# Kernel tuning notes

Hardware: AMD Instinct MI355X
Metric: run time of the kernel (lower is better)

Reference implementation:

```python
import jax, jax.numpy as jnp
import numpy as np

B, S, C, H = 8, 1024, 768, 8
D = C // H  # head dim = 96
MLP = 4 * C


def setup_inputs() -> dict:
    key = jax.random.key(0)
    ks = jax.random.split(key, 12)
    sc = 0.02
    return {
        "x": jax.random.normal(ks[0], (B, S, C), jnp.float32),
        "ln1_w": jnp.ones((S, C), jnp.float32),
        "ln1_b": jnp.zeros((S, C), jnp.float32),
        "ln2_w": jnp.ones((S, C), jnp.float32),
        "ln2_b": jnp.zeros((S, C), jnp.float32),
        "qkv_w": jax.random.normal(ks[1], (C, 3 * C), jnp.float32) * sc,
        "proj_w": jax.random.normal(ks[2], (C, C), jnp.float32) * sc,
        "mlp_w1": jax.random.normal(ks[3], (C, MLP), jnp.float32) * sc,
        "mlp_b1": jnp.zeros((MLP,), jnp.float32),
        "mlp_w2": jax.random.normal(ks[4], (MLP, C), jnp.float32) * sc,
        "mlp_b2": jnp.zeros((C,), jnp.float32),
    }


def _layernorm2d(x, w, b, eps=1e-5):
    # normalizes over BOTH (seq, channel) dims, per nn.LayerNorm([length, channel])
    mu = jnp.mean(x, axis=(-2, -1), keepdims=True)
    var = jnp.mean(jnp.square(x - mu), axis=(-2, -1), keepdims=True)
    return (x - mu) * jax.lax.rsqrt(var + eps) * w + b


def _attention(x, qkv_w, proj_w):
    b, s, _ = x.shape
    qkv = (x @ qkv_w).reshape(b, s, 3, H, D)
    q, k, v = qkv[:, :, 0], qkv[:, :, 1], qkv[:, :, 2]  # [b, s, h, d]
    # NOTE: original module applies NO 1/sqrt(d) scaling
    scores = jnp.einsum("bshd,bthd->bhst", q, k)
    attn = jax.nn.softmax(scores, axis=-1)
    out = jnp.einsum("bhst,bthd->bshd", attn, v).reshape(b, s, C)
    return out @ proj_w


def reference(x, ln1_w, ln1_b, ln2_w, ln2_b, qkv_w, proj_w, mlp_w1, mlp_b1, mlp_w2, mlp_b2):
    # dropout is identity in eval mode
    h = x + _attention(_layernorm2d(x, ln1_w, ln1_b), qkv_w, proj_w)
    y = _layernorm2d(h, ln2_w, ln2_b)
    y = jax.nn.gelu(y @ mlp_w1 + mlp_b1, approximate=False)
    return h + (y @ mlp_w2 + mlp_b2)
```

## Files before the change

### kernel.cpp

```cpp
#include <hip/hip_runtime.h>
#include <hip/hip_bf16.h>

#define S_LEN 1024
#define NB 8
#define NC 768
#define NH 8
#define HD 96
#define NMLP 3072
#define SC (S_LEN*NC)
#define BS (NB*S_LEN)

typedef __attribute__((ext_vector_type(8))) unsigned short u16x8;
typedef __attribute__((ext_vector_type(4))) unsigned short u16x4;
typedef __attribute__((ext_vector_type(8))) __bf16 bf16x8;
typedef __attribute__((ext_vector_type(4))) float f32x4;

__device__ __forceinline__ unsigned short f2b(float f) {
  union { __hip_bfloat16 h; unsigned short u; } cvt;
  cvt.h = __float2bfloat16(f);
  return cvt.u;
}

__device__ __forceinline__ void gload16(const unsigned short* g, unsigned short* l) {
  __builtin_amdgcn_global_load_lds(
      (const __attribute__((address_space(1))) unsigned int*)g,
      (__attribute__((address_space(3))) unsigned int*)l, 16, 0, 0);
}

template<int EPI>
__global__ __launch_bounds__(256, 2)
void gemm_bt(const unsigned short* __restrict__ A, int lda,
             const unsigned short* __restrict__ Bt, int ldb,
             void* __restrict__ Cv, int ldc,
             int K,
             const float* __restrict__ bias,
             const float* __restrict__ residual, int ldr)
{
  __shared__ unsigned short As[128*32];
  __shared__ unsigned short Bs[128*32];
  const int tid = threadIdx.x;
  const int lane = tid & 63;
  const int wid = tid >> 6;
  const int wm = wid & 1, wn = wid >> 1;
  const int r15 = lane & 15, g = lane >> 4;
  const int tm = blockIdx.x * 128;
  const int tn = blockIdx.y * 128;

  const unsigned short* Ab = A  + (size_t)(tm + wid*32 + (lane>>2))*lda + (lane&3)*8;
  const unsigned short* Bb = Bt + (size_t)(tn + wid*32 + (lane>>2))*ldb + (lane&3)*8;

  f32x4 acc[4][4];
  #pragma unroll
  for (int m = 0; m < 4; ++m)
    #pragma unroll
    for (int n = 0; n < 4; ++n)
      acc[m][n] = (f32x4){0.f, 0.f, 0.f, 0.f};

  for (int k0 = 0; k0 < K; k0 += 32) {
    gload16(Ab + k0,                    As + (wid*2 + 0)*512);
    gload16(Ab + (size_t)16*lda + k0,   As + (wid*2 + 1)*512);
    gload16(Bb + k0,                    Bs + (wid*2 + 0)*512);
    gload16(Bb + (size_t)16*ldb + k0,   Bs + (wid*2 + 1)*512);
    __syncthreads();
    bf16x8 af[4], bfr[4];
    #pragma unroll
    for (int m = 0; m < 4; ++m)
      af[m] = *(const bf16x8*)(As + (wm*64 + m*16 + r15)*32 + g*8);
    #pragma unroll
    for (int n = 0; n < 4; ++n)
      bfr[n] = *(const bf16x8*)(Bs + (wn*64 + n*16 + r15)*32 + g*8);
    #pragma unroll
    for (int m = 0; m < 4; ++m)
      #pragma unroll
      for (int n = 0; n < 4; ++n)
        acc[m][n] = __builtin_amdgcn_mfma_f32_16x16x32_bf16(af[m], bfr[n], acc[m][n], 0, 0, 0);
    __syncthreads();
  }

  unsigned short* Cu = (unsigned short*)Cv;
  float* Cf = (float*)Cv;
  #pragma unroll
  for (int m = 0; m < 4; ++m) {
    #pragma unroll
    for (int n = 0; n < 4; ++n) {
      const int col = tn + wn*64 + n*16 + r15;
      #pragma unroll
      for (int r = 0; r < 4; ++r) {
        const int row = tm + wm*64 + m*16 + g*4 + r;
        float v = acc[m][n][r];
        if (EPI == 2 || EPI == 4) v += bias[col];
        if (EPI == 3 || EPI == 4) v += residual[(size_t)row*ldr + col];
        if (EPI == 2) v = 0.5f*v*(1.0f + erff(v*0.70710678118654752f));
        if (EPI == 0 || EPI == 2) Cu[(size_t)row*ldc + col] = f2b(v);
        else                      Cf[(size_t)row*ldc + col] = v;
      }
    }
  }
}

__global__ __launch_bounds__(256, 2)
void flash_attn(const unsigned short* __restrict__ qkv,
                const unsigned short* __restrict__ vt,
                unsigned short* __restrict__ outb)
{
  __shared__ unsigned short Ks[128*96];
  __shared__ unsigned short Vs[96*128];
  __shared__ unsigned short Ps[128*128];
  const int tid = threadIdx.x, lane = tid & 63, wq = tid >> 6;
  const int r15 = lane & 15, g = lane >> 4;
  const int bh = blockIdx.y, b = bh >> 3, h = bh & 7;
  const int q0 = blockIdx.x * 128;
  const int swz = (r15 & 7) << 4;
  char* PsB = (char*)Ps;
  char* VsB = (char*)Vs;

  bf16x8 qf[2][3];
  {
    const unsigned short* qb = qkv + ((size_t)b*S_LEN + q0 + wq*32 + r15)*2304 + h*HD + g*8;
    #pragma unroll
    for (int n = 0; n < 2; ++n)
      #pragma unroll
      for (int kc = 0; kc < 3; ++kc)
        qf[n][kc] = *(const bf16x8*)(qb + (size_t)n*16*2304 + kc*32);
  }

  int krow[6], kcol[6], vrow[6], vcol[6];
  #pragma unroll
  for (int i = 0; i < 6; ++i) {
    const int c = (wq*6 + i)*64 + lane;
    krow[i] = c / 12;
    kcol[i] = (c % 12) * 8;
    const int L = c * 16;
    const int row = L >> 8, cb = L & 255;
    vrow[i] = row;
    vcol[i] = (cb ^ ((row & 7) << 4)) >> 1;
  }
  const unsigned short* kbase = qkv + (size_t)b*S_LEN*2304 + NC + h*HD;
  const unsigned short* vbase = vt + (size_t)bh*HD*S_LEN;

  f32x4 oacc[6][2];
  #pragma unroll
  for (int m = 0; m < 6; ++m) {
    oacc[m][0] = (f32x4){0.f,0.f,0.f,0.f};
    oacc[m][1] = (f32x4){0.f,0.f,0.f,0.f};
  }
  float mrun[2] = {-INFINITY, -INFINITY};
  float lrun[2] = {0.f, 0.f};

  for (int kt = 0; kt < 8; ++kt) {
    const unsigned short* ksrc = kbase + (size_t)kt*128*2304;
    const unsigned short* vsrc = vbase + kt*128;
    #pragma unroll
    for (int i = 0; i < 6; ++i) {
      gload16(ksrc + (size_t)krow[i]*2304 + kcol[i], Ks + (wq*6 + i)*512);
      gload16(vsrc + vrow[i]*1024 + vcol[i],         Vs + (wq*6 + i)*512);
    }
    __syncthreads();

    f32x4 sacc[8][2];
    #pragma unroll
    for (int m = 0; m < 8; ++m) {
      sacc[m][0] = (f32x4){0.f,0.f,0.f,0.f};
      sacc[m][1] = (f32x4){0.f,0.f,0.f,0.f};
    }
    #pragma unroll
    for (int kc = 0; kc < 3; ++kc)
      #pragma unroll
      for (int m = 0; m < 8; ++m) {
        bf16x8 kf = *(const bf16x8*)(Ks + (m*16 + r15)*96 + kc*32 + g*8);
        sacc[m][0] = __builtin_amdgcn_mfma_f32_16x16x32_bf16(kf, qf[0][kc], sacc[m][0], 0,0,0);
        sacc[m][1] = __builtin_amdgcn_mfma_f32_16x16x32_bf16(kf, qf[1][kc], sacc[m][1], 0,0,0);
      }

    #pragma unroll
    for (int n = 0; n < 2; ++n) {
      float pm = -INFINITY;
      #pragma unroll
      for (int m = 0; m < 8; ++m)
        #pragma unroll
        for (int r = 0; r < 4; ++r) pm = fmaxf(pm, sacc[m][n][r]);
      pm = fmaxf(pm, __shfl_xor(pm, 16));
      pm = fmaxf(pm, __shfl_xor(pm, 32));
      const float newm = fmaxf(mrun[n], pm);
      const float scale = __expf(mrun[n] - newm);
      mrun[n] = newm;
      const int qloc = wq*32 + n*16 + r15;
      float s = 0.f;
      #pragma unroll
      for (int m = 0; m < 8; ++m) {
        float e0 = __expf(sacc[m][n][0] - newm);
        float e1 = __expf(sacc[m][n][1] - newm);
        float e2 = __expf(sacc[m][n][2] - newm);
        float e3 = __expf(sacc[m][n][3] - newm);
        s += (e0 + e1) + (e2 + e3);
        u16x4 pk = { f2b(e0), f2b(e1), f2b(e2), f2b(e3) };
        *(u16x4*)(PsB + ((qloc*256 + m*32 + g*8) ^ swz)) = pk;
      }
      s += __shfl_xor(s, 16);
      s += __shfl_xor(s, 32);
      lrun[n] = lrun[n]*scale + s;
      #pragma unroll
      for (int m = 0; m < 6; ++m) oacc[m][n] *= scale;
    }

    #pragma unroll
    for (int kc = 0; kc < 4; ++kc) {
      bf16x8 pf0 = *(const bf16x8*)(PsB + (((wq*32      + r15)*256 + kc*64 + g*16) ^ swz));
      bf16x8 pf1 = *(const bf16x8*)(PsB + (((wq*32 + 16 + r15)*256 + kc*64 + g*16) ^ swz));
      #pragma unroll
      for (int m = 0; m < 6; ++m) {
        bf16x8 vf = *(const bf16x8*)(VsB + (((m*16 + r15)*256 + kc*64 + g*16) ^ swz));
        oacc[m][0] = __builtin_amdgcn_mfma_f32_16x16x32_bf16(vf, pf0, oacc[m][0], 0,0,0);
        oacc[m][1] = __builtin_amdgcn_mfma_f32_16x16x32_bf16(vf, pf1, oacc[m][1], 0,0,0);
      }
    }
    __syncthreads();
  }

  #pragma unroll
  for (int n = 0; n < 2; ++n) {
    const float inv = 1.0f / lrun[n];
    unsigned short* orow = outb + ((size_t)b*S_LEN + q0 + wq*32 + n*16 + r15)*NC + h*HD;
    #pragma unroll
    for (int m = 0; m < 6; ++m) {
      u16x4 pk = { f2b(oacc[m][n][0]*inv), f2b(oacc[m][n][1]*inv),
                   f2b(oacc[m][n][2]*inv), f2b(oacc[m][n][3]*inv) };
      *(u16x4*)(orow + m*16 + g*4) = pk;
    }
  }
}

__global__ void transpose_cast(const float* __restrict__ W, unsigned short* __restrict__ Wt,
                               int K, int N)
{
  __shared__ float tile[32][33];
  const int tx = threadIdx.x & 31, ty = threadIdx.x >> 5;
  const int n0 = blockIdx.x * 32, k0 = blockIdx.y * 32;
  #pragma unroll
  for (int i = 0; i < 32; i += 8)
    tile[ty + i][tx] = W[(size_t)(k0 + ty + i)*N + n0 + tx];
  __syncthreads();
  #pragma unroll
  for (int i = 0; i < 32; i += 8)
    Wt[(size_t)(n0 + ty + i)*K + k0 + tx] = f2b(tile[tx][ty + i]);
}

__global__ void transpose_v(const unsigned short* __restrict__ qkv, unsigned short* __restrict__ vt)
{
  __shared__ unsigned short tile[32][33];
  const int bh = blockIdx.z, b = bh >> 3, h = bh & 7;
  const unsigned short* v = qkv + (size_t)b*S_LEN*3*NC + 2*NC + h*HD;
  unsigned short* o = vt + (size_t)bh*HD*S_LEN;
  const int s0 = blockIdx.x * 32, d0 = blockIdx.y * 32;
  const int tx = threadIdx.x & 31, ty = threadIdx.x >> 5;
  #pragma unroll
  for (int i = 0; i < 32; i += 8)
    tile[ty + i][tx] = v[(size_t)(s0 + ty + i)*(3*NC) + d0 + tx];
  __syncthreads();
  #pragma unroll
  for (int i = 0; i < 32; i += 8)
    o[(size_t)(d0 + ty + i)*S_LEN + s0 + tx] = tile[tx][ty + i];
}

__global__ void ln_part(const float* __restrict__ X, float* __restrict__ part)
{
  const int b = blockIdx.x / 96, blk = blockIdx.x % 96;
  const float4* xb = (const float4*)(X + (size_t)b*SC);
  float s = 0.f, s2 = 0.f;
  #pragma unroll
  for (int i = 0; i < 8; ++i) {
    float4 v = xb[blk*2048 + i*256 + threadIdx.x];
    s  += v.x + v.y + v.z + v.w;
    s2 += v.x*v.x + v.y*v.y + v.z*v.z + v.w*v.w;
  }
  #pragma unroll
  for (int o = 32; o; o >>= 1) { s += __shfl_down(s, o); s2 += __shfl_down(s2, o); }
  __shared__ float r1[4], r2[4];
  const int w = threadIdx.x >> 6;
  if ((threadIdx.x & 63) == 0) { r1[w] = s; r2[w] = s2; }
  __syncthreads();
  if (threadIdx.x == 0) {
    part[(b*96 + blk)*2]     = r1[0] + r1[1] + r1[2] + r1[3];
    part[(b*96 + blk)*2 + 1] = r2[0] + r2[1] + r2[2] + r2[3];
  }
}

__global__ void ln_fin(const float* __restrict__ part, float* __restrict__ stats)
{
  const int b = blockIdx.x;
  float s = 0.f, s2 = 0.f;
  for (int i = threadIdx.x; i < 96; i += 64) {
    s  += part[(b*96 + i)*2];
    s2 += part[(b*96 + i)*2 + 1];
  }
  #pragma unroll
  for (int o = 32; o; o >>= 1) { s += __shfl_down(s, o); s2 += __shfl_down(s2, o); }
  if (threadIdx.x == 0) {
    const float inv = 1.0f / (float)SC;
    const float mu = s * inv;
    const float var = s2 * inv - mu*mu;
    stats[b*2] = mu;
    stats[b*2 + 1] = rsqrtf(var + 1e-5f);
  }
}

__global__ void ln_apply(const float* __restrict__ X, const float* __restrict__ W,
                         const float* __restrict__ Bv, const float* __restrict__ stats,
                         unsigned short* __restrict__ out)
{
  const size_t i = ((size_t)blockIdx.x*256 + threadIdx.x) * 8;
  const int b = (int)(i / SC);
  const size_t r = i % SC;
  const float mu = stats[b*2], rs = stats[b*2 + 1];
  float4 x0 = *(const float4*)(X + i),  x1 = *(const float4*)(X + i + 4);
  float4 w0 = *(const float4*)(W + r),  w1 = *(const float4*)(W + r + 4);
  float4 b0 = *(const float4*)(Bv + r), b1 = *(const float4*)(Bv + r + 4);
  u16x8 o;
  o[0] = f2b((x0.x - mu)*rs*w0.x + b0.x);
  o[1] = f2b((x0.y - mu)*rs*w0.y + b0.y);
  o[2] = f2b((x0.z - mu)*rs*w0.z + b0.z);
  o[3] = f2b((x0.w - mu)*rs*w0.w + b0.w);
  o[4] = f2b((x1.x - mu)*rs*w1.x + b1.x);
  o[5] = f2b((x1.y - mu)*rs*w1.y + b1.y);
  o[6] = f2b((x1.z - mu)*rs*w1.z + b1.z);
  o[7] = f2b((x1.w - mu)*rs*w1.w + b1.w);
  *(u16x8*)(out + i) = o;
}

extern "C" void kernel_launch(void* const* d_in, const int* in_sizes, int n_in,
                              void* d_out, int out_size, void* d_ws, size_t ws_size,
                              hipStream_t stream) {
  const float* x      = (const float*)d_in[0];
  const float* ln1_w  = (const float*)d_in[1];
  const float* ln1_b  = (const float*)d_in[2];
  const float* ln2_w  = (const float*)d_in[3];
  const float* ln2_b  = (const float*)d_in[4];
  const float* qkv_w  = (const float*)d_in[5];
  const float* proj_w = (const float*)d_in[6];
  const float* mlp_w1 = (const float*)d_in[7];
  const float* mlp_b1 = (const float*)d_in[8];
  const float* mlp_w2 = (const float*)d_in[9];
  const float* mlp_b2 = (const float*)d_in[10];
  float* out = (float*)d_out;

  char* ws = (char*)d_ws;
  size_t off = 0;
  auto alloc = [&](size_t b) { size_t o = off; off += (b + 255) & ~(size_t)255; return o; };
  unsigned short* wqkvT  = (unsigned short*)(ws + alloc((size_t)3*NC*NC*2));
  unsigned short* wprojT = (unsigned short*)(ws + alloc((size_t)NC*NC*2));
  unsigned short* w1T    = (unsigned short*)(ws + alloc((size_t)NMLP*NC*2));
  unsigned short* w2T    = (unsigned short*)(ws + alloc((size_t)NC*NMLP*2));
  unsigned short* lnbf   = (unsigned short*)(ws + alloc((size_t)BS*NC*2));
  const size_t qkvOff    = alloc((size_t)BS*3*NC*2);
  unsigned short* qkvbf  = (unsigned short*)(ws + qkvOff);
  unsigned short* vt     = (unsigned short*)(ws + alloc((size_t)NB*NH*HD*S_LEN*2));
  unsigned short* ybf    = (unsigned short*)(ws + qkvOff);
  float* hbuf            = (float*)(ws + alloc((size_t)BS*NC*4));
  float* part            = (float*)(ws + alloc((size_t)NB*96*2*4));
  float* stats           = (float*)(ws + alloc((size_t)NB*2*4));
  (void)ws_size; (void)in_sizes; (void)n_in; (void)out_size;

  const dim3 blk(256);

  transpose_cast<<<dim3(3*NC/32, NC/32),   blk, 0, stream>>>(qkv_w,  wqkvT,  NC, 3*NC);
  transpose_cast<<<dim3(NC/32, NC/32),     blk, 0, stream>>>(proj_w, wprojT, NC, NC);
  transpose_cast<<<dim3(NMLP/32, NC/32),   blk, 0, stream>>>(mlp_w1, w1T,    NC, NMLP);
  transpose_cast<<<dim3(NC/32, NMLP/32),   blk, 0, stream>>>(mlp_w2, w2T,    NMLP, NC);

  ln_part<<<dim3(NB*96), blk, 0, stream>>>(x, part);
  ln_fin<<<dim3(NB), dim3(64), 0, stream>>>(part, stats);
  ln_apply<<<dim3(BS*NC/2048), blk, 0, stream>>>(x, ln1_w, ln1_b, stats, lnbf);

  gemm_bt<0><<<dim3(BS/128, 3*NC/128), blk, 0, stream>>>(
      lnbf, NC, wqkvT, NC, qkvbf, 3*NC, NC, nullptr, nullptr, 0);

  transpose_v<<<dim3(S_LEN/32, HD/32, NB*NH), blk, 0, stream>>>(qkvbf, vt);

  flash_attn<<<dim3(S_LEN/128, NB*NH), blk, 0, stream>>>(qkvbf, vt, lnbf);

  gemm_bt<3><<<dim3(BS/128, NC/128), blk, 0, stream>>>(
      lnbf, NC, wprojT, NC, hbuf, NC, NC, nullptr, x, NC);

  ln_part<<<dim3(NB*96), blk, 0, stream>>>(hbuf, part);
  ln_fin<<<dim3(NB), dim3(64), 0, stream>>>(part, stats);
  ln_apply<<<dim3(BS*NC/2048), blk, 0, stream>>>(hbuf, ln2_w, ln2_b, stats, lnbf);

  gemm_bt<2><<<dim3(BS/128, NMLP/128), blk, 0, stream>>>(
      lnbf, NC, w1T, NC, ybf, NMLP, NC, mlp_b1, nullptr, 0);

  gemm_bt<4><<<dim3(BS/128, NC/128), blk, 0, stream>>>(
      ybf, NMLP, w2T, NMLP, out, NC, NMLP, mlp_b2, hbuf, NC);
}
```

Before: 298.9 us.

## Replace GEMM with 8-wave 128x256 triple-buffered pipelined kernel and tanh GELU

Replaces the single-buffered 128x128 GEMM with a 512-thread kernel on a 128x256 tile and K-steps of 64. It uses a three-stage LDS ring with XOR-swizzled layout, and staggers global-to-LDS prefetches between MFMA groups under s_setprio. This is meant to hide global load latency and LDS bank conflicts, and to drop one barrier per K step. The erf-based GELU epilogue becomes a tanh approximation, and flash attention MFMA loops gain setprio hints. The trade-offs are more LDS use, one block per CU, and slight numeric deviation from exact GELU.

Result: slower. 325.0 us (+8.7%).

```diff
diff --git a/kernel.cpp b/kernel.cpp
--- a/kernel.cpp
+++ b/kernel.cpp
@@ -27,27 +27,48 @@
       (__attribute__((address_space(3))) unsigned int*)l, 16, 0, 0);
 }
 
+__device__ __forceinline__ float gelu_f(float v) {
+  float u = v * (0.7978845608f + 0.0356774081f * v * v);
+  float au = fabsf(u);
+  float e = __expf(-2.0f * au);
+  float th = (1.0f - e) / (1.0f + e);
+  th = copysignf(th, u);
+  return 0.5f * v * (1.0f + th);
+}
+
 template<int EPI>
-__global__ __launch_bounds__(256, 2)
-void gemm_bt(const unsigned short* __restrict__ A, int lda,
-             const unsigned short* __restrict__ Bt, int ldb,
-             void* __restrict__ Cv, int ldc,
-             int K,
-             const float* __restrict__ bias,
-             const float* __restrict__ residual, int ldr)
-{
-  __shared__ unsigned short As[128*32];
-  __shared__ unsigned short Bs[128*32];
-  const int tid = threadIdx.x;
-  const int lane = tid & 63;
-  const int wid = tid >> 6;
+__global__ __launch_bounds__(512, 1)
+void gemm8(const unsigned short* __restrict__ A, int lda,
+           const unsigned short* __restrict__ Bt, int ldb,
+           void* __restrict__ Cv, int ldc, int K,
+           const float* __restrict__ bias,
+           const float* __restrict__ residual, int ldr)
+{
+  __shared__ unsigned short As[3*8192];
+  __shared__ unsigned short Bs[3*16384];
+  const int tid = threadIdx.x, lane = tid & 63, wid = tid >> 6;
   const int wm = wid & 1, wn = wid >> 1;
   const int r15 = lane & 15, g = lane >> 4;
-  const int tm = blockIdx.x * 128;
-  const int tn = blockIdx.y * 128;
-
-  const unsigned short* Ab = A  + (size_t)(tm + wid*32 + (lane>>2))*lda + (lane&3)*8;
-  const unsigned short* Bb = Bt + (size_t)(tn + wid*32 + (lane>>2))*ldb + (lane&3)*8;
+  const int tm = blockIdx.x * 128, tn = blockIdx.y * 256;
+  const int NT = K >> 6;
+
+  const int srow = lane >> 3;
+  const int scol = ((lane & 7) ^ srow) << 3;
+  const unsigned short* Ag = A  + (size_t)(tm + wid*8 + srow)*lda + scol;
+  const unsigned short* Bg = Bt + (size_t)(tn + wid*8 + srow)*ldb + scol;
+
+  const int kx  = (r15 & 7) << 4;
+  const int k0b = (g*16) ^ kx;
+  const int k1b = (64 + g*16) ^ kx;
+  char* AsB = (char*)As;
+  char* BsB = (char*)Bs;
+  const int arow = (wm*64 + r15) * 128;
+  const int brow = (wn*64 + r15) * 128;
+
+#define LDA8(m,ks) (*(const bf16x8*)(AsB + bufA + arow + (m)*2048 + ((ks) ? k1b : k0b)))
+#define LDB8(n,ks) (*(const bf16x8*)(BsB + bufB + brow + (n)*2048 + ((ks) ? k1b : k0b)))
+#define STGA(j,kk,bf) gload16(Ag + (size_t)((j)*64)*lda + (kk), As + (bf)*8192  + (j)*4096 + wid*512)
+#define STGB(j,kk,bf) gload16(Bg + (size_t)((j)*64)*ldb + (kk), Bs + (bf)*16384 + (j)*4096 + wid*512)
 
   f32x4 acc[4][4];
   #pragma unroll
@@ -56,26 +77,80 @@
     for (int n = 0; n < 4; ++n)
       acc[m][n] = (f32x4){0.f, 0.f, 0.f, 0.f};
 
-  for (int k0 = 0; k0 < K; k0 += 32) {
-    gload16(Ab + k0,                    As + (wid*2 + 0)*512);
-    gload16(Ab + (size_t)16*lda + k0,   As + (wid*2 + 1)*512);
-    gload16(Bb + k0,                    Bs + (wid*2 + 0)*512);
-    gload16(Bb + (size_t)16*ldb + k0,   Bs + (wid*2 + 1)*512);
-    __syncthreads();
-    bf16x8 af[4], bfr[4];
-    #pragma unroll
-    for (int m = 0; m < 4; ++m)
-      af[m] = *(const bf16x8*)(As + (wm*64 + m*16 + r15)*32 + g*8);
-    #pragma unroll
-    for (int n = 0; n < 4; ++n)
-      bfr[n] = *(const bf16x8*)(Bs + (wn*64 + n*16 + r15)*32 + g*8);
-    #pragma unroll
-    for (int m = 0; m < 4; ++m)
-      #pragma unroll
-      for (int n = 0; n < 4; ++n)
-        acc[m][n] = __builtin_amdgcn_mfma_f32_16x16x32_bf16(af[m], bfr[n], acc[m][n], 0, 0, 0);
-    __syncthreads();
-  }
+  STGA(0,0,0); STGA(1,0,0); STGB(0,0,0); STGB(1,0,0); STGB(2,0,0); STGB(3,0,0);
+  STGA(0,64,1); STGA(1,64,1); STGB(0,64,1); STGB(1,64,1); STGB(2,64,1); STGB(3,64,1);
+  asm volatile("s_waitcnt vmcnt(6)" ::: "memory");
+  __builtin_amdgcn_s_barrier();
+
+  int buf = 0, nbuf = 2;
+  for (int t = 0; t < NT; ++t) {
+    const int kk = (t + 2) << 6;
+    const bool pre = (t + 2) < NT;
+    const int bufA = buf * 16384;
+    const int bufB = buf * 32768;
+    bf16x8 a0[2][2], a1[2][2], b0[2][2], b1[2][2];
+
+    if (pre) { STGA(0,kk,nbuf); STGA(1,kk,nbuf); }
+    #pragma unroll
+    for (int m = 0; m < 2; ++m) { a0[m][0] = LDA8(m,0); a0[m][1] = LDA8(m,1); }
+    #pragma unroll
+    for (int n = 0; n < 2; ++n) { b0[n][0] = LDB8(n,0); b0[n][1] = LDB8(n,1); }
+    __builtin_amdgcn_s_setprio(1);
+    #pragma unroll
+    for (int m = 0; m < 2; ++m)
+      #pragma unroll
+      for (int n = 0; n < 2; ++n) {
+        acc[m][n] = __builtin_amdgcn_mfma_f32_16x16x32_bf16(a0[m][0], b0[n][0], acc[m][n], 0,0,0);
+        acc[m][n] = __builtin_amdgcn_mfma_f32_16x16x32_bf16(a0[m][1], b0[n][1], acc[m][n], 0,0,0);
+      }
+    __builtin_amdgcn_s_setprio(0);
+
+    if (pre) { STGB(0,kk,nbuf); STGB(1,kk,nbuf); }
+    #pragma unroll
+    for (int n = 0; n < 2; ++n) { b1[n][0] = LDB8(n+2,0); b1[n][1] = LDB8(n+2,1); }
+    __builtin_amdgcn_s_setprio(1);
+    #pragma unroll
+    for (int m = 0; m < 2; ++m)
+      #pragma unroll
+      for (int n = 0; n < 2; ++n) {
+        acc[m][n+2] = __builtin_amdgcn_mfma_f32_16x16x32_bf16(a0[m][0], b1[n][0], acc[m][n+2], 0,0,0);
+        acc[m][n+2] = __builtin_amdgcn_mfma_f32_16x16x32_bf16(a0[m][1], b1[n][1], acc[m][n+2], 0,0,0);
+      }
+    __builtin_amdgcn_s_setprio(0);
+
+    if (pre) { STGB(2,kk,nbuf); STGB(3,kk,nbuf); }
+    #pragma unroll
+    for (int m = 0; m < 2; ++m) { a1[m][0] = LDA8(m+2,0); a1[m][1] = LDA8(m+2,1); }
+    __builtin_amdgcn_s_setprio(1);
+    #pragma unroll
+    for (int m = 0; m < 2; ++m)
+      #pragma unroll
+      for (int n = 0; n < 2; ++n) {
+        acc[m+2][n+2] = __builtin_amdgcn_mfma_f32_16x16x32_bf16(a1[m][0], b1[n][0], acc[m+2][n+2], 0,0,0);
+        acc[m+2][n+2] = __builtin_amdgcn_mfma_f32_16x16x32_bf16(a1[m][1], b1[n][1], acc[m+2][n+2], 0,0,0);
+      }
+    __builtin_amdgcn_s_setprio(0);
+
+    __builtin_amdgcn_s_setprio(1);
+    #pragma unroll
+    for (int m = 0; m < 2; ++m)
+      #pragma unroll
+      for (int n = 0; n < 2; ++n) {
+        acc[m+2][n] = __builtin_amdgcn_mfma_f32_16x16x32_bf16(a1[m][0], b0[n][0], acc[m+2][n], 0,0,0);
+        acc[m+2][n] = __builtin_amdgcn_mfma_f32_16x16x32_bf16(a1[m][1], b0[n][1], acc[m+2][n], 0,0,0);
+      }
+    __builtin_amdgcn_s_setprio(0);
+
+    if (pre) asm volatile("s_waitcnt vmcnt(6)" ::: "memory");
+    else     asm volatile("s_waitcnt vmcnt(0)" ::: "memory");
+    __builtin_amdgcn_s_barrier();
+    buf  = (buf  == 2) ? 0 : buf  + 1;
+    nbuf = (nbuf == 2) ? 0 : nbuf + 1;
+  }
+#undef LDA8
+#undef LDB8
+#undef STGA
+#undef STGB
 
   unsigned short* Cu = (unsigned short*)Cv;
   float* Cf = (float*)Cv;
@@ -90,7 +165,7 @@
         float v = acc[m][n][r];
         if (EPI == 2 || EPI == 4) v += bias[col];
         if (EPI == 3 || EPI == 4) v += residual[(size_t)row*ldr + col];
-        if (EPI == 2) v = 0.5f*v*(1.0f + erff(v*0.70710678118654752f));
+        if (EPI == 2) v = gelu_f(v);
         if (EPI == 0 || EPI == 2) Cu[(size_t)row*ldc + col] = f2b(v);
         else                      Cf[(size_t)row*ldc + col] = v;
       }
@@ -163,6 +238,7 @@
       sacc[m][0] = (f32x4){0.f,0.f,0.f,0.f};
       sacc[m][1] = (f32x4){0.f,0.f,0.f,0.f};
     }
+    __builtin_amdgcn_s_setprio(1);
     #pragma unroll
     for (int kc = 0; kc < 3; ++kc)
       #pragma unroll
@@ -171,6 +247,7 @@
         sacc[m][0] = __builtin_amdgcn_mfma_f32_16x16x32_bf16(kf, qf[0][kc], sacc[m][0], 0,0,0);
         sacc[m][1] = __builtin_amdgcn_mfma_f32_16x16x32_bf16(kf, qf[1][kc], sacc[m][1], 0,0,0);
       }
+    __builtin_amdgcn_s_setprio(0);
 
     #pragma unroll
     for (int n = 0; n < 2; ++n) {
@@ -207,12 +284,14 @@
     for (int kc = 0; kc < 4; ++kc) {
       bf16x8 pf0 = *(const bf16x8*)(PsB + (((wq*32      + r15)*256 + kc*64 + g*16) ^ swz));
       bf16x8 pf1 = *(const bf16x8*)(PsB + (((wq*32 + 16 + r15)*256 + kc*64 + g*16) ^ swz));
+      __builtin_amdgcn_s_setprio(1);
       #pragma unroll
       for (int m = 0; m < 6; ++m) {
         bf16x8 vf = *(const bf16x8*)(VsB + (((m*16 + r15)*256 + kc*64 + g*16) ^ swz));
         oacc[m][0] = __builtin_amdgcn_mfma_f32_16x16x32_bf16(vf, pf0, oacc[m][0], 0,0,0);
         oacc[m][1] = __builtin_amdgcn_mfma_f32_16x16x32_bf16(vf, pf1, oacc[m][1], 0,0,0);
       }
+      __builtin_amdgcn_s_setprio(0);
     }
     __syncthreads();
   }
@@ -361,6 +440,7 @@
   (void)ws_size; (void)in_sizes; (void)n_in; (void)out_size;
 
   const dim3 blk(256);
+  const dim3 blk512(512);
 
   transpose_cast<<<dim3(3*NC/32, NC/32),   blk, 0, stream>>>(qkv_w,  wqkvT,  NC, 3*NC);
   transpose_cast<<<dim3(NC/32, NC/32),     blk, 0, stream>>>(proj_w, wprojT, NC, NC);
@@ -371,23 +451,23 @@
   ln_fin<<<dim3(NB), dim3(64), 0, stream>>>(part, stats);
   ln_apply<<<dim3(BS*NC/2048), blk, 0, stream>>>(x, ln1_w, ln1_b, stats, lnbf);
 
-  gemm_bt<0><<<dim3(BS/128, 3*NC/128), blk, 0, stream>>>(
+  gemm8<0><<<dim3(BS/128, 3*NC/256), blk512, 0, stream>>>(
       lnbf, NC, wqkvT, NC, qkvbf, 3*NC, NC, nullptr, nullptr, 0);
 
   transpose_v<<<dim3(S_LEN/32, HD/32, NB*NH), blk, 0, stream>>>(qkvbf, vt);
 
   flash_attn<<<dim3(S_LEN/128, NB*NH), blk, 0, stream>>>(qkvbf, vt, lnbf);
 
-  gemm_bt<3><<<dim3(BS/128, NC/128), blk, 0, stream>>>(
+  gemm8<3><<<dim3(BS/128, NC/256), blk512, 0, stream>>>(
       lnbf, NC, wprojT, NC, hbuf, NC, NC, nullptr, x, NC);
 
   ln_part<<<dim3(NB*96), blk, 0, stream>>>(hbuf, part);
   ln_fin<<<dim3(NB), dim3(64), 0, stream>>>(part, stats);
   ln_apply<<<dim3(BS*NC/2048), blk, 0, stream>>>(hbuf, ln2_w, ln2_b, stats, lnbf);
 
-  gemm_bt<2><<<dim3(BS/128, NMLP/128), blk, 0, stream>>>(
+  gemm8<2><<<dim3(BS/128, NMLP/256), blk512, 0, stream>>>(
       lnbf, NC, w1T, NC, ybf, NMLP, NC, mlp_b1, nullptr, 0);
 
-  gemm_bt<4><<<dim3(BS/128, NC/128), blk, 0, stream>>>(
+  gemm8<4><<<dim3(BS/128, NC/256), blk512, 0, stream>>>(
       ybf, NMLP, w2T, NMLP, out, NC, NMLP, mlp_b2, hbuf, NC);
 }
```
